# Kernel optimization log

Measured on AMD Instinct MI355X. Metric: run time of the kernel, lower is better.

## Reference

```python
import jax, jax.numpy as jnp
import numpy as np

NUM_Q_HEADS = 16
NUM_KV_HEADS = 4
GROUP_SIZE = NUM_Q_HEADS // NUM_KV_HEADS  # 4
GROUP_DIM = 128                           # head dim, also RoPE dim
THETA = 10000.0


def _rope_cos_sin(num_tokens, dim, dtype):
    # freqs = 1/theta^(2i/d); angles[t, i] = t * freqs[i]
    inv_freq = 1.0 / (THETA ** (jnp.arange(0, dim, 2, dtype=jnp.float32) / dim))
    t = jnp.arange(num_tokens, dtype=jnp.float32)
    angles = jnp.outer(t, inv_freq)  # [N, d/2]
    # broadcast to [N, 1, 1, d/2] to match q/k shape [B, N, gs, kvh, d/2]
    cos = jnp.cos(angles)[:, None, None, :].astype(dtype)
    sin = jnp.sin(angles)[:, None, None, :].astype(dtype)
    return cos, sin


def _apply_rope(x, cos, sin):
    # x: [B, N, gs, kvh, d]; complex rotation on interleaved (even, odd) pairs
    xr = x.reshape(*x.shape[:-1], -1, 2)
    xe, xo = xr[..., 0], xr[..., 1]
    oe = xe * cos - xo * sin
    oo = xe * sin + xo * cos
    return jnp.stack([oe, oo], axis=-1).reshape(x.shape)


def setup_inputs() -> dict:
    key = jax.random.key(0)
    ks = jax.random.split(key, 5)
    B, N, D = 1, 2048, 2048
    KV_D = GROUP_DIM * NUM_KV_HEADS  # 512
    s = 0.02
    return {
        "x": jax.random.normal(ks[0], (B, N, D), dtype=jnp.float32),
        "Wq": jax.random.normal(ks[1], (D, D), dtype=jnp.float32) * s,
        "Wk": jax.random.normal(ks[2], (D, KV_D), dtype=jnp.float32) * s,
        "Wv": jax.random.normal(ks[3], (D, KV_D), dtype=jnp.float32) * s,
        "Wo": jax.random.normal(ks[4], (D, D), dtype=jnp.float32) * s,
    }


def reference(x, Wq, Wk, Wv, Wo):
    B, N, D = x.shape
    d = GROUP_DIM
    # projections
    q = (x @ Wq).reshape(B, N, GROUP_SIZE, NUM_KV_HEADS, d)
    k = (x @ Wk).reshape(B, N, 1, NUM_KV_HEADS, d)
    v = (x @ Wv).reshape(B, N, 1, NUM_KV_HEADS, d)
    # RoPE (interleaved complex rotation)
    cos, sin = _rope_cos_sin(N, d, x.dtype)
    q = _apply_rope(q, cos, sin)
    k = _apply_rope(k, cos, sin)
    # to [B, kvh, gs, N, d] / [B, kvh, N, d]
    q = jnp.transpose(q, (0, 3, 2, 1, 4))        # b k s n d
    k = jnp.transpose(k[:, :, 0], (0, 2, 1, 3))  # b k m d
    v = jnp.transpose(v[:, :, 0], (0, 2, 1, 3))  # b k m d
    scores = jnp.einsum('bksnd,bkmd->bksnm', q, k)
    causal = jnp.tril(jnp.ones((N, N), dtype=bool))
    scores = jnp.where(causal, scores, -jnp.inf)
    weights = jax.nn.softmax(scores / jnp.sqrt(jnp.asarray(d, x.dtype)), axis=-1)
    ctx = jnp.einsum('bksnm,bkmd->bksnd', weights, v)   # [B, kvh, gs, N, d]
    # flatten heads (kvh-major, matching torch flatten(1,2)), then [B, N, D]
    ctx = ctx.reshape(B, NUM_KV_HEADS * GROUP_SIZE, N, d)
    ctx = jnp.transpose(ctx, (0, 2, 1, 3)).reshape(B, N, D)
    return ctx @ Wo
```

## Files before the change

### kernel.cpp

```cpp
#include <hip/hip_runtime.h>

typedef unsigned short u16;
typedef float f32x4 __attribute__((ext_vector_type(4)));
typedef short s16x8 __attribute__((ext_vector_type(8)));
typedef short s16x4 __attribute__((ext_vector_type(4)));

__device__ __forceinline__ u16 f2b(float f) {
  union { float f; unsigned u; } v; v.f = f;
  unsigned r = v.u + 0x7fffu + ((v.u >> 16) & 1u);
  return (u16)(r >> 16);
}
__device__ __forceinline__ float b2f(u16 b) {
  union { unsigned u; float f; } v; v.u = ((unsigned)b) << 16;
  return v.f;
}
__device__ __forceinline__ f32x4 mfma_bf16(s16x8 a, s16x8 b, f32x4 c) {
  return __builtin_amdgcn_mfma_f32_16x16x32_bf16(a, b, c, 0, 0, 0);
}
__device__ __forceinline__ void gl_lds16(const u16* g, u16* l) {
  __builtin_amdgcn_global_load_lds(
      (const __attribute__((address_space(1))) void*)g,
      (__attribute__((address_space(3))) void*)l, 16, 0, 0);
}

__global__ void conv_x(const float* __restrict__ in, u16* __restrict__ out, int n) {
  int i = (blockIdx.x * 256 + threadIdx.x) * 8;
  if (i >= n) return;
  f32x4 a = *(const f32x4*)(in + i);
  f32x4 b = *(const f32x4*)(in + i + 4);
  s16x8 o = {(short)f2b(a.x), (short)f2b(a.y), (short)f2b(a.z), (short)f2b(a.w),
             (short)f2b(b.x), (short)f2b(b.y), (short)f2b(b.z), (short)f2b(b.w)};
  *(s16x8*)(out + i) = o;
}

__global__ void transW_qkv(const float* __restrict__ Wq, const float* __restrict__ Wk,
                           const float* __restrict__ Wv, u16* __restrict__ WqkvT) {
  __shared__ u16 tile[64][68];
  const int ox = blockIdx.x * 64;
  const int oy = blockIdx.y * 64;
  const float* src; int scol, C;
  if (ox < 2048)      { src = Wq; scol = ox;        C = 2048; }
  else if (ox < 2560) { src = Wk; scol = ox - 2048; C = 512;  }
  else                { src = Wv; scol = ox - 2560; C = 512;  }
  const int t = threadIdx.x, lr = t >> 4, c4 = (t & 15) * 4;
#pragma unroll
  for (int p = 0; p < 4; ++p) {
    int r = p * 16 + lr;
    f32x4 v = *(const f32x4*)(src + (size_t)(oy + r) * C + scol + c4);
    s16x4 pk = {(short)f2b(v.x), (short)f2b(v.y), (short)f2b(v.z), (short)f2b(v.w)};
    *(s16x4*)(&tile[r][c4]) = pk;
  }
  __syncthreads();
#pragma unroll
  for (int q = 0; q < 4; ++q) {
    int oc = q * 16 + lr;
    s16x4 pk = {(short)tile[c4 + 0][oc], (short)tile[c4 + 1][oc],
                (short)tile[c4 + 2][oc], (short)tile[c4 + 3][oc]};
    *(s16x4*)(WqkvT + (size_t)(ox + oc) * 2048 + oy + c4) = pk;
  }
}

__global__ void transW_o(const float* __restrict__ Wo, u16* __restrict__ WoT) {
  __shared__ u16 tile[64][68];
  const int ox = blockIdx.x * 64, oy = blockIdx.y * 64;
  const int t = threadIdx.x, lr = t >> 4, c4 = (t & 15) * 4;
#pragma unroll
  for (int p = 0; p < 4; ++p) {
    int r = p * 16 + lr;
    f32x4 v = *(const f32x4*)(Wo + (size_t)(oy + r) * 2048 + ox + c4);
    s16x4 pk = {(short)f2b(v.x), (short)f2b(v.y), (short)f2b(v.z), (short)f2b(v.w)};
    *(s16x4*)(&tile[r][c4]) = pk;
  }
  __syncthreads();
#pragma unroll
  for (int q = 0; q < 4; ++q) {
    int oc = q * 16 + lr;
    s16x4 pk = {(short)tile[c4 + 0][oc], (short)tile[c4 + 1][oc],
                (short)tile[c4 + 2][oc], (short)tile[c4 + 3][oc]};
    *(s16x4*)(WoT + (size_t)(ox + oc) * 2048 + oy + c4) = pk;
  }
}

__global__ void transpose_v(const u16* __restrict__ qkv, u16* __restrict__ vT) {
  __shared__ u16 tile[64][68];
  const int bx = blockIdx.x * 64, by = blockIdx.y * 64;
  const int t = threadIdx.x, lr = t >> 4, c4 = (t & 15) * 4;
#pragma unroll
  for (int p = 0; p < 4; ++p) {
    int r = p * 16 + lr;
    s16x4 v = *(const s16x4*)(qkv + (size_t)(by + r) * 3072 + 2560 + bx + c4);
    *(s16x4*)(&tile[r][c4]) = v;
  }
  __syncthreads();
#pragma unroll
  for (int q = 0; q < 4; ++q) {
    int oc = q * 16 + lr;
    s16x4 pk = {(short)tile[c4 + 0][oc], (short)tile[c4 + 1][oc],
                (short)tile[c4 + 2][oc], (short)tile[c4 + 3][oc]};
    *(s16x4*)(vT + (size_t)(bx + oc) * 2048 + by + c4) = pk;
  }
}

__device__ __forceinline__ void gemm_core(const u16* __restrict__ A,
                                          const u16* __restrict__ Bt,
                                          int kbeg, int kend, int K,
                                          int m0, int n0,
                                          f32x4 (*acc)[4], u16* As, u16* Bs) {
  const int t = threadIdx.x;
  const int wave = t >> 6, lane = t & 63, quad = lane >> 4, lc = lane & 15;
  const int wm = (wave >> 1) * 64, wn = (wave & 1) * 64;
  for (int k0 = kbeg; k0 < kend; k0 += 32) {
#pragma unroll
    for (int h = 0; h < 2; ++h) {
      int ch = h * 256 + t, row = ch >> 2, kc = (ch & 3) * 8;
      gl_lds16(A  + (size_t)(m0 + row) * K + k0 + kc, As + (size_t)(h * 256 + wave * 64) * 8);
      gl_lds16(Bt + (size_t)(n0 + row) * K + k0 + kc, Bs + (size_t)(h * 256 + wave * 64) * 8);
    }
    __syncthreads();
    s16x8 af[4], bfr[4];
#pragma unroll
    for (int i = 0; i < 4; ++i)
      af[i] = *(const s16x8*)(As + (wm + i * 16 + lc) * 32 + quad * 8);
#pragma unroll
    for (int j = 0; j < 4; ++j)
      bfr[j] = *(const s16x8*)(Bs + (wn + j * 16 + lc) * 32 + quad * 8);
#pragma unroll
    for (int i = 0; i < 4; ++i)
#pragma unroll
      for (int j = 0; j < 4; ++j)
        acc[i][j] = mfma_bf16(af[i], bfr[j], acc[i][j]);
    __syncthreads();
  }
}

__global__ __launch_bounds__(256, 2) void gemm_qkv_half(const u16* __restrict__ A,
                                                        const u16* __restrict__ Bt,
                                                        u16* __restrict__ P) {
  __shared__ __align__(16) u16 As[128 * 32];
  __shared__ __align__(16) u16 Bs[128 * 32];
  const int kh = blockIdx.z;
  const int n0 = blockIdx.x * 128, m0 = blockIdx.y * 128;
  const int lane = threadIdx.x & 63, wave = threadIdx.x >> 6;
  const int quad = lane >> 4, lc = lane & 15;
  const int wm = (wave >> 1) * 64, wn = (wave & 1) * 64;
  const f32x4 z = {0.f, 0.f, 0.f, 0.f};
  f32x4 acc[4][4];
#pragma unroll
  for (int i = 0; i < 4; ++i)
#pragma unroll
    for (int j = 0; j < 4; ++j) acc[i][j] = z;
  gemm_core(A, Bt, kh * 1024, kh * 1024 + 1024, 2048, m0, n0, acc, As, Bs);
  u16* Pk = P + (size_t)kh * (2048 * 3072);
#pragma unroll
  for (int i = 0; i < 4; ++i)
#pragma unroll
    for (int j = 0; j < 4; ++j)
#pragma unroll
      for (int r = 0; r < 4; ++r)
        Pk[(size_t)(m0 + wm + i * 16 + quad * 4 + r) * 3072 + n0 + wn + j * 16 + lc] =
            f2b(acc[i][j][r]);
}

__global__ void reduce_rope(const u16* __restrict__ P, u16* __restrict__ qkv) {
  const int lin = blockIdx.x * 256 + threadIdx.x;
  const int row = lin / 384, c8 = (lin - row * 384) * 8;
  const u16* p0 = P + (size_t)row * 3072 + c8;
  s16x8 a = *(const s16x8*)p0;
  s16x8 b = *(const s16x8*)(p0 + 6291456);
  float v[8];
#pragma unroll
  for (int i = 0; i < 8; ++i) v[i] = b2f((u16)a[i]) + b2f((u16)b[i]);
  if (c8 < 2560) {
#pragma unroll
    for (int h = 0; h < 4; ++h) {
      const int i = 2 * h;
      const int ip = ((c8 + i) & 127) >> 1;
      const float ang = (float)row * exp2f(-0.20762050593046014f * (float)ip);
      float sv, cv;
      sincosf(ang, &sv, &cv);
      const float e = v[i], o = v[i + 1];
      v[i]     = e * cv - o * sv;
      v[i + 1] = e * sv + o * cv;
    }
  }
  s16x8 o;
#pragma unroll
  for (int i = 0; i < 8; ++i) o[i] = (short)f2b(v[i]);
  *(s16x8*)(qkv + (size_t)row * 3072 + c8) = o;
}

__global__ __launch_bounds__(256, 2) void gemm_out_half(const u16* __restrict__ A,
                                                        const u16* __restrict__ Bt,
                                                        u16* __restrict__ Po) {
  __shared__ __align__(16) u16 As[128 * 32];
  __shared__ __align__(16) u16 Bs[128 * 32];
  const int kh = blockIdx.z;
  const int n0 = blockIdx.x * 128, m0 = blockIdx.y * 128;
  const int lane = threadIdx.x & 63, wave = threadIdx.x >> 6;
  const int quad = lane >> 4, lc = lane & 15;
  const int wm = (wave >> 1) * 64, wn = (wave & 1) * 64;
  const f32x4 z = {0.f, 0.f, 0.f, 0.f};
  f32x4 acc[4][4];
#pragma unroll
  for (int i = 0; i < 4; ++i)
#pragma unroll
    for (int j = 0; j < 4; ++j) acc[i][j] = z;
  gemm_core(A, Bt, kh * 1024, kh * 1024 + 1024, 2048, m0, n0, acc, As, Bs);
  u16* Pk = Po + (size_t)kh * (2048 * 2048);
#pragma unroll
  for (int i = 0; i < 4; ++i)
#pragma unroll
    for (int j = 0; j < 4; ++j)
#pragma unroll
      for (int r = 0; r < 4; ++r)
        Pk[(size_t)(m0 + wm + i * 16 + quad * 4 + r) * 2048 + n0 + wn + j * 16 + lc] =
            f2b(acc[i][j][r]);
}

__global__ void reduce_out(const u16* __restrict__ Po, float* __restrict__ out) {
  const int lin = blockIdx.x * 256 + threadIdx.x;
  const u16* p0 = Po + (size_t)lin * 8;
  s16x8 a = *(const s16x8*)p0;
  s16x8 b = *(const s16x8*)(p0 + 4194304);
  f32x4 o0, o1;
#pragma unroll
  for (int i = 0; i < 4; ++i) o0[i] = b2f((u16)a[i]) + b2f((u16)b[i]);
#pragma unroll
  for (int i = 0; i < 4; ++i) o1[i] = b2f((u16)a[i + 4]) + b2f((u16)b[i + 4]);
  *(f32x4*)(out + (size_t)lin * 8) = o0;
  *(f32x4*)(out + (size_t)lin * 8 + 4) = o1;
}

__global__ __launch_bounds__(256, 2) void attn_k(const u16* __restrict__ qkv,
                                                 const u16* __restrict__ vT,
                                                 u16* __restrict__ Opart,
                                                 float* __restrict__ Lpart) {
  const int bid = blockIdx.x;
  const int hq = bid / 40, idx = bid % 40;
  int qt, c;
  if (idx < 4)       { qt = idx;                          c = 0; }
  else if (idx < 12) { int w = idx - 4;  qt = 4 + (w >> 1);  c = w & 1; }
  else if (idx < 24) { int w = idx - 12; qt = 8 + w / 3;     c = w % 3; }
  else               { int w = idx - 24; qt = 12 + (w >> 2); c = w & 3; }
  const int s0 = c * 8;
  const int s1 = min(c * 8 + 8, 2 * qt + 2);

  const int kvh = hq & 3;
  const int qc0 = hq << 7, kc0 = 2048 + (kvh << 7), vr0 = kvh << 7;

  __shared__ __align__(16) u16 Ks[64 * 136];
  __shared__ __align__(16) u16 Vs[128 * 72];
  __shared__ __align__(16) u16 Ps[128 * 72];

  const int t = threadIdx.x, wave = t >> 6, lane = t & 63;
  const int quad = lane >> 4, lc = lane & 15;
  const int kr = t >> 4, kc = (t & 15) * 8;
  const int vr = t >> 3, vc = (t & 7) * 8;

  s16x8 qf[2][4];
#pragma unroll
  for (int i = 0; i < 2; ++i)
#pragma unroll
    for (int ks = 0; ks < 4; ++ks)
      qf[i][ks] = *(const s16x8*)(qkv +
          (size_t)(qt * 128 + wave * 32 + i * 16 + lc) * 3072 +
          qc0 + ks * 32 + quad * 8);

  const f32x4 z = {0.f, 0.f, 0.f, 0.f};
  f32x4 oa[2][8];
#pragma unroll
  for (int i = 0; i < 2; ++i)
#pragma unroll
    for (int n = 0; n < 8; ++n) oa[i][n] = z;
  float Ls[2][4] = {{0.f, 0.f, 0.f, 0.f}, {0.f, 0.f, 0.f, 0.f}};
  const float scale2 = 0.12751744545f;

  s16x8 kpf[4], vpf[4];
  {
    const int j0 = s0 * 64;
#pragma unroll
    for (int p = 0; p < 4; ++p)
      kpf[p] = *(const s16x8*)(qkv + (size_t)(j0 + p * 16 + kr) * 3072 + kc0 + kc);
#pragma unroll
    for (int p = 0; p < 4; ++p)
      vpf[p] = *(const s16x8*)(vT + (size_t)(vr0 + p * 32 + vr) * 2048 + j0 + vc);
  }

  for (int tile = s0; tile < s1; ++tile) {
    const int j0 = tile * 64;
    __syncthreads();
#pragma unroll
    for (int p = 0; p < 4; ++p)
      *(s16x8*)(Ks + (p * 16 + kr) * 136 + kc) = kpf[p];
#pragma unroll
    for (int p = 0; p < 4; ++p)
      *(s16x8*)(Vs + (p * 32 + vr) * 72 + vc) = vpf[p];
    __syncthreads();
    if (tile + 1 < s1) {
      const int j1 = j0 + 64;
#pragma unroll
      for (int p = 0; p < 4; ++p)
        kpf[p] = *(const s16x8*)(qkv + (size_t)(j1 + p * 16 + kr) * 3072 + kc0 + kc);
#pragma unroll
      for (int p = 0; p < 4; ++p)
        vpf[p] = *(const s16x8*)(vT + (size_t)(vr0 + p * 32 + vr) * 2048 + j1 + vc);
    }
    f32x4 sa[2][4];
#pragma unroll
    for (int i = 0; i < 2; ++i)
#pragma unroll
      for (int n = 0; n < 4; ++n) sa[i][n] = z;
#pragma unroll
    for (int ks = 0; ks < 4; ++ks)
#pragma unroll
      for (int n = 0; n < 4; ++n) {
        s16x8 bf = *(const s16x8*)(Ks + (n * 16 + lc) * 136 + ks * 32 + quad * 8);
        sa[0][n] = mfma_bf16(qf[0][ks], bf, sa[0][n]);
        sa[1][n] = mfma_bf16(qf[1][ks], bf, sa[1][n]);
      }
#pragma unroll
    for (int i = 0; i < 2; ++i) {
      const int qrow_base = qt * 128 + wave * 32 + i * 16 + quad * 4;
#pragma unroll
      for (int n = 0; n < 4; ++n) {
        int jc = j0 + n * 16 + lc;
#pragma unroll
        for (int r = 0; r < 4; ++r) {
          float e = (jc <= qrow_base + r) ? exp2f(sa[i][n][r] * scale2) : 0.f;
          Ps[(wave * 32 + i * 16 + quad * 4 + r) * 72 + n * 16 + lc] = f2b(e);
          Ls[i][r] += e;
        }
      }
    }
#pragma unroll
    for (int ks = 0; ks < 2; ++ks)
#pragma unroll
      for (int i = 0; i < 2; ++i) {
        s16x8 af = *(const s16x8*)(Ps + (wave * 32 + i * 16 + lc) * 72 +
                                   ks * 32 + quad * 8);
#pragma unroll
        for (int n = 0; n < 8; ++n) {
          s16x8 bf = *(const s16x8*)(Vs + (n * 16 + lc) * 72 + ks * 32 + quad * 8);
          oa[i][n] = mfma_bf16(af, bf, oa[i][n]);
        }
      }
  }
#pragma unroll
  for (int i = 0; i < 2; ++i)
#pragma unroll
    for (int r = 0; r < 4; ++r) {
      float s = Ls[i][r];
      s += __shfl_xor(s, 1);
      s += __shfl_xor(s, 2);
      s += __shfl_xor(s, 4);
      s += __shfl_xor(s, 8);
      Ls[i][r] = s;
    }
  u16* Ob = Opart + (size_t)bid * (128 * 128);
  if (lc == 0) {
#pragma unroll
    for (int i = 0; i < 2; ++i)
#pragma unroll
      for (int r = 0; r < 4; ++r)
        Lpart[(size_t)bid * 128 + wave * 32 + i * 16 + quad * 4 + r] = Ls[i][r];
  }
#pragma unroll
  for (int i = 0; i < 2; ++i)
#pragma unroll
    for (int n = 0; n < 8; ++n)
#pragma unroll
      for (int r = 0; r < 4; ++r)
        Ob[(wave * 32 + i * 16 + quad * 4 + r) * 128 + n * 16 + lc] =
            f2b(oa[i][n][r]);
}

__global__ void attn_combine(const u16* __restrict__ Opart,
                             const float* __restrict__ Lpart,
                             u16* __restrict__ ctx) {
  const int hq = blockIdx.y, kvh = hq & 3, sg = hq >> 2;
  const int lin = blockIdx.x * 256 + threadIdx.x;
  const int token = lin >> 4, d8 = (lin & 15) << 3;
  const int qt = token >> 7, row = token & 127;
  const int tier = qt >> 2;
  const int btab[4] = {0, 4, 12, 24};
  const int base = hq * 40 + btab[tier] + (qt & 3) * (tier + 1);
  const int cnt = tier + 1;
  float acc[8] = {0.f, 0.f, 0.f, 0.f, 0.f, 0.f, 0.f, 0.f};
  float L = 0.f;
  for (int c = 0; c < cnt; ++c) {
    const int b = base + c;
    L += Lpart[(size_t)b * 128 + row];
    s16x8 o = *(const s16x8*)(Opart + (size_t)b * 16384 + row * 128 + d8);
#pragma unroll
    for (int i = 0; i < 8; ++i) acc[i] += b2f((u16)o[i]);
  }
  const float inv = 1.f / L;
  s16x8 out;
#pragma unroll
  for (int i = 0; i < 8; ++i) out[i] = (short)f2b(acc[i] * inv);
  *(s16x8*)(ctx + (size_t)token * 2048 + ((kvh * 4 + sg) << 7) + d8) = out;
}

extern "C" void kernel_launch(void* const* d_in, const int* in_sizes, int n_in,
                              void* d_out, int out_size, void* d_ws, size_t ws_size,
                              hipStream_t stream) {
  const float* x  = (const float*)d_in[0];
  const float* Wq = (const float*)d_in[1];
  const float* Wk = (const float*)d_in[2];
  const float* Wv = (const float*)d_in[3];
  const float* Wo = (const float*)d_in[4];

  char* base = (char*)d_ws;
  u16*   xb    = (u16*)(base);
  u16*   qkvb  = (u16*)(base);
  u16*   WoT   = (u16*)(base);
  u16*   WqkvT = (u16*)(base + 8388608);
  u16*   vTb   = (u16*)(base + 12582912);
  float* Lpart = (float*)(base + 14680064);
  u16*   Pq    = (u16*)(base + 20971520);
  u16*   Opart = (u16*)(base + 20971520);
  u16*   Po    = (u16*)(base + 20971520);
  u16*   ctxb  = (u16*)(base + 41943040);

  conv_x<<<2048, 256, 0, stream>>>(x, xb, 2048 * 2048);
  transW_qkv<<<dim3(48, 32), 256, 0, stream>>>(Wq, Wk, Wv, WqkvT);

  gemm_qkv_half<<<dim3(24, 16, 2), 256, 0, stream>>>(xb, WqkvT, Pq);
  reduce_rope<<<3072, 256, 0, stream>>>(Pq, qkvb);

  transpose_v<<<dim3(8, 32), 256, 0, stream>>>(qkvb, vTb);

  attn_k<<<640, 256, 0, stream>>>(qkvb, vTb, Opart, Lpart);
  attn_combine<<<dim3(128, 16), 256, 0, stream>>>(Opart, Lpart, ctxb);

  transW_o<<<dim3(32, 32), 256, 0, stream>>>(Wo, WoT);
  gemm_out_half<<<dim3(16, 16, 2), 256, 0, stream>>>(ctxb, WoT, Po);
  reduce_out<<<2048, 256, 0, stream>>>(Po, (float*)d_out);
}
```

Before: 238.4 us.

## Swizzle attention LDS tiles, reverse block order, add mask-free softmax path

Replaces the padded LDS layouts for K, V and P tiles with XOR-swizzled unpadded layouts to avoid bank conflicts and shrink shared memory. It raises the occupancy hint to three blocks per CU and reverses the block-to-work mapping so the heavier late query tiles start first, with the combine kernel's indexing updated to match. It also adds a fast path that skips causal masking for fully visible tiles, and raises wave priority around the MFMA sections. The risks are register pressure from the higher occupancy target and the extra index arithmetic added by the swizzle.

```diff
diff --git a/kernel.cpp b/kernel.cpp
--- a/kernel.cpp
+++ b/kernel.cpp
@@ -22,6 +22,8 @@
       (const __attribute__((address_space(1))) void*)g,
       (__attribute__((address_space(3))) void*)l, 16, 0, 0);
 }
+__device__ __forceinline__ int kswz(int r, int c) { return ((r << 7) + c) ^ ((r & 7) << 3); }
+__device__ __forceinline__ int vswz(int r, int c) { return ((r << 6) + c) ^ ((r & 7) << 3); }
 
 __global__ void conv_x(const float* __restrict__ in, u16* __restrict__ out, int n) {
   int i = (blockIdx.x * 256 + threadIdx.x) * 8;
@@ -231,12 +233,12 @@
   *(f32x4*)(out + (size_t)lin * 8 + 4) = o1;
 }
 
-__global__ __launch_bounds__(256, 2) void attn_k(const u16* __restrict__ qkv,
+__global__ __launch_bounds__(256, 3) void attn_k(const u16* __restrict__ qkv,
                                                  const u16* __restrict__ vT,
                                                  u16* __restrict__ Opart,
                                                  float* __restrict__ Lpart) {
   const int bid = blockIdx.x;
-  const int hq = bid / 40, idx = bid % 40;
+  const int hq = bid / 40, idx = 39 - (bid % 40);
   int qt, c;
   if (idx < 4)       { qt = idx;                          c = 0; }
   else if (idx < 12) { int w = idx - 4;  qt = 4 + (w >> 1);  c = w & 1; }
@@ -248,9 +250,9 @@
   const int kvh = hq & 3;
   const int qc0 = hq << 7, kc0 = 2048 + (kvh << 7), vr0 = kvh << 7;
 
-  __shared__ __align__(16) u16 Ks[64 * 136];
-  __shared__ __align__(16) u16 Vs[128 * 72];
-  __shared__ __align__(16) u16 Ps[128 * 72];
+  __shared__ __align__(16) u16 Ks[64 * 128];
+  __shared__ __align__(16) u16 Vs[128 * 64];
+  __shared__ __align__(16) u16 Ps[128 * 64];
 
   const int t = threadIdx.x, wave = t >> 6, lane = t & 63;
   const int quad = lane >> 4, lc = lane & 15;
@@ -291,10 +293,10 @@
     __syncthreads();
 #pragma unroll
     for (int p = 0; p < 4; ++p)
-      *(s16x8*)(Ks + (p * 16 + kr) * 136 + kc) = kpf[p];
+      *(s16x8*)(Ks + kswz(p * 16 + kr, kc)) = kpf[p];
 #pragma unroll
     for (int p = 0; p < 4; ++p)
-      *(s16x8*)(Vs + (p * 32 + vr) * 72 + vc) = vpf[p];
+      *(s16x8*)(Vs + vswz(p * 32 + vr, vc)) = vpf[p];
     __syncthreads();
     if (tile + 1 < s1) {
       const int j1 = j0 + 64;
@@ -310,40 +312,57 @@
     for (int i = 0; i < 2; ++i)
 #pragma unroll
       for (int n = 0; n < 4; ++n) sa[i][n] = z;
+    __builtin_amdgcn_s_setprio(1);
 #pragma unroll
     for (int ks = 0; ks < 4; ++ks)
 #pragma unroll
       for (int n = 0; n < 4; ++n) {
-        s16x8 bf = *(const s16x8*)(Ks + (n * 16 + lc) * 136 + ks * 32 + quad * 8);
+        s16x8 bf = *(const s16x8*)(Ks + kswz(n * 16 + lc, ks * 32 + quad * 8));
         sa[0][n] = mfma_bf16(qf[0][ks], bf, sa[0][n]);
         sa[1][n] = mfma_bf16(qf[1][ks], bf, sa[1][n]);
       }
-#pragma unroll
-    for (int i = 0; i < 2; ++i) {
-      const int qrow_base = qt * 128 + wave * 32 + i * 16 + quad * 4;
-#pragma unroll
-      for (int n = 0; n < 4; ++n) {
-        int jc = j0 + n * 16 + lc;
-#pragma unroll
-        for (int r = 0; r < 4; ++r) {
-          float e = (jc <= qrow_base + r) ? exp2f(sa[i][n][r] * scale2) : 0.f;
-          Ps[(wave * 32 + i * 16 + quad * 4 + r) * 72 + n * 16 + lc] = f2b(e);
-          Ls[i][r] += e;
+    __builtin_amdgcn_s_setprio(0);
+    if (j0 + 64 <= qt * 128) {
+#pragma unroll
+      for (int i = 0; i < 2; ++i)
+#pragma unroll
+        for (int n = 0; n < 4; ++n)
+#pragma unroll
+          for (int r = 0; r < 4; ++r) {
+            float e = exp2f(sa[i][n][r] * scale2);
+            Ps[vswz(wave * 32 + i * 16 + quad * 4 + r, n * 16 + lc)] = f2b(e);
+            Ls[i][r] += e;
+          }
+    } else {
+#pragma unroll
+      for (int i = 0; i < 2; ++i) {
+        const int qrow_base = qt * 128 + wave * 32 + i * 16 + quad * 4;
+#pragma unroll
+        for (int n = 0; n < 4; ++n) {
+          int jc = j0 + n * 16 + lc;
+#pragma unroll
+          for (int r = 0; r < 4; ++r) {
+            float e = (jc <= qrow_base + r) ? exp2f(sa[i][n][r] * scale2) : 0.f;
+            Ps[vswz(wave * 32 + i * 16 + quad * 4 + r, n * 16 + lc)] = f2b(e);
+            Ls[i][r] += e;
+          }
         }
       }
     }
+    __builtin_amdgcn_s_setprio(1);
 #pragma unroll
     for (int ks = 0; ks < 2; ++ks)
 #pragma unroll
       for (int i = 0; i < 2; ++i) {
-        s16x8 af = *(const s16x8*)(Ps + (wave * 32 + i * 16 + lc) * 72 +
-                                   ks * 32 + quad * 8);
+        s16x8 af = *(const s16x8*)(Ps + vswz(wave * 32 + i * 16 + lc,
+                                             ks * 32 + quad * 8));
 #pragma unroll
         for (int n = 0; n < 8; ++n) {
-          s16x8 bf = *(const s16x8*)(Vs + (n * 16 + lc) * 72 + ks * 32 + quad * 8);
+          s16x8 bf = *(const s16x8*)(Vs + vswz(n * 16 + lc, ks * 32 + quad * 8));
           oa[i][n] = mfma_bf16(af, bf, oa[i][n]);
         }
       }
+    __builtin_amdgcn_s_setprio(0);
   }
 #pragma unroll
   for (int i = 0; i < 2; ++i)
@@ -383,12 +402,12 @@
   const int qt = token >> 7, row = token & 127;
   const int tier = qt >> 2;
   const int btab[4] = {0, 4, 12, 24};
-  const int base = hq * 40 + btab[tier] + (qt & 3) * (tier + 1);
+  const int base = btab[tier] + (qt & 3) * (tier + 1);
   const int cnt = tier + 1;
   float acc[8] = {0.f, 0.f, 0.f, 0.f, 0.f, 0.f, 0.f, 0.f};
   float L = 0.f;
   for (int c = 0; c < cnt; ++c) {
-    const int b = base + c;
+    const int b = hq * 40 + (39 - (base + c));
     L += Lpart[(size_t)b * 128 + row];
     s16x8 o = *(const s16x8*)(Opart + (size_t)b * 16384 + row * 128 + d8);
 #pragma unroll
```

Result: slower. 431.0 us (+80.7%).
